# Optimization experiments

Hardware: AMD Instinct MI355X
Metric: run time of the kernel (lower is better)

The kernel has to match this reference:

```python
import jax, jax.numpy as jnp
import numpy as np

N, E, B = 150000, 600000, 1024
F_IN, F_HID = 78, 312          # 78 * 2**output_dim_power_0(=2)
OUT_DIM = 128
L, VOCAB, EMB = 1000, 26, 128  # num_features_xt+1 = 26 embedding rows
NF, KS = 8, 8                  # 2**n_filters_power, 2**kernel_size_power
CONV_FLAT = NF * (EMB - KS + 1)  # 8*121 = 968
K_HOPS = 2
SLOPE = 0.01                   # torch leaky_relu default

def _lin(k, i, o):
    s = 1.0 / np.sqrt(i)
    kw, kb = jax.random.split(k)
    return (jax.random.uniform(kw, (i, o), jnp.float32, -s, s),
            jax.random.uniform(kb, (o,), jnp.float32, -s, s))

def setup_inputs() -> dict:
    key = jax.random.key(0)
    ks = jax.random.split(key, 12)
    x = jax.random.normal(ks[0], (N, F_IN), jnp.float32)
    edge_index = jax.random.randint(ks[1], (2, E), 0, N)
    batch = (jnp.arange(N) * B) // N            # sorted graph ids, all B graphs nonempty
    target = jax.random.randint(ks[2], (B, L), 0, VOCAB)
    sgc_w, sgc_b = _lin(ks[3], F_IN, F_HID)
    fcg1_w, fcg1_b = _lin(ks[4], F_HID, OUT_DIM)
    emb_table = jax.random.normal(ks[5], (VOCAB, EMB), jnp.float32)
    sc = 1.0 / np.sqrt(L * KS)
    conv_w = jax.random.uniform(ks[6], (NF, L, KS), jnp.float32, -sc, sc)  # OIW
    conv_b = jax.random.uniform(ks[7], (NF,), jnp.float32, -sc, sc)
    fcxt_w, fcxt_b = _lin(ks[8], CONV_FLAT, OUT_DIM)
    fc1_w, fc1_b = _lin(ks[9], 2 * OUT_DIM, 1024)
    fc2_w, fc2_b = _lin(ks[10], 1024, 512)
    out_w, out_b = _lin(ks[11], 512, 1)
    return dict(x=x, sgc_w=sgc_w, sgc_b=sgc_b, fcg1_w=fcg1_w, fcg1_b=fcg1_b,
                emb_table=emb_table, conv_w=conv_w, conv_b=conv_b,
                fcxt_w=fcxt_w, fcxt_b=fcxt_b, fc1_w=fc1_w, fc1_b=fc1_b,
                fc2_w=fc2_w, fc2_b=fc2_b, out_w=out_w, out_b=out_b,
                edge_index=edge_index, batch=batch, target=target)

def reference(x, sgc_w, sgc_b, fcg1_w, fcg1_b, emb_table, conv_w, conv_b,
              fcxt_w, fcxt_b, fc1_w, fc1_b, fc2_w, fc2_b, out_w, out_b,
              edge_index, batch, target):
    # --- SGConv: K-hop symmetric-normalized propagation with self-loops, then linear ---
    loop = jnp.arange(N)
    src = jnp.concatenate([edge_index[0], loop])
    dst = jnp.concatenate([edge_index[1], loop])
    deg = jax.ops.segment_sum(jnp.ones_like(src, jnp.float32), dst, num_segments=N)
    dinv = jnp.where(deg > 0, jax.lax.rsqrt(deg), 0.0)
    norm = (dinv[src] * dinv[dst])[:, None]
    h = x
    for _ in range(K_HOPS):
        h = jax.ops.segment_sum(h[src] * norm, dst, num_segments=N)  # [N, F]
    h = jax.nn.leaky_relu(h @ sgc_w + sgc_b, SLOPE)                  # [N, 312]
    # --- global max pool per graph + fc_g1 ---
    g = jax.ops.segment_max(h, batch, num_segments=B)                # [B, 312]
    g = jax.nn.leaky_relu(g @ fcg1_w + fcg1_b, SLOPE)                # [B, 128]
    # --- protein branch: embed -> Conv1d(in=1000) over embed axis -> flatten -> fc ---
    emb = emb_table[target]                                          # [B, 1000, 128]
    conv = jax.lax.conv_general_dilated(emb, conv_w, (1,), 'VALID',
                                        dimension_numbers=('NCW', 'OIW', 'NCW'))
    conv = conv + conv_b[None, :, None]                              # [B, 8, 121]
    xt = conv.reshape(B, CONV_FLAT) @ fcxt_w + fcxt_b                # [B, 128]
    # --- head ---
    xc = jnp.concatenate([g, xt], axis=1)                            # [B, 256]
    xc = jax.nn.relu(xc @ fc1_w + fc1_b)
    xc = jax.nn.relu(xc @ fc2_w + fc2_b)
    return xc @ out_w + out_b                                        # [B, 1]
```

## Files before the change

kernel.cpp:

```cpp
#include <hip/hip_runtime.h>

#define N_NODES 150000
#define N_EDGES 600000
#define BATCH   1024
#define F_IN    78
#define F_HID   312
#define OUT_DIMW 128
#define SEQ_L   1000
#define VOCAB   26
#define EMB     128
#define NF      8
#define KS      8
#define CONV_WO 121
#define CONV_FLAT 968
#define SK      208
#define SLOPE   0.01f
#define KEY_NEGMAX ((int)0x80800000)
#define SCAN_NBLK ((N_NODES + 255) / 256)

#define KPU  96
#define NT   20
#define BSW_HALF (3 * NT * 64 * 8)
#define M_PAD 150016
#define HA_PLANE ((size_t)M_PAD * KPU)

typedef __attribute__((ext_vector_type(8))) short bf8;
typedef __attribute__((ext_vector_type(4))) float f4;

__device__ __forceinline__ short f2bf(float f) {
  unsigned u = __float_as_uint(f);
  return (short)((u + 0x7fffu + ((u >> 16) & 1u)) >> 16);
}
__device__ __forceinline__ float bf2f(short h) {
  return __uint_as_float(((unsigned)(unsigned short)h) << 16);
}

__device__ __forceinline__ int fkey(float v) {
  int i = __float_as_int(v);
  return i >= 0 ? i : (i ^ 0x7fffffff);
}
__device__ __forceinline__ float fdec(int k) {
  return __int_as_float(k >= 0 ? k : (k ^ 0x7fffffff));
}

__global__ void k_zero_i(int* __restrict__ p, int n) {
  int i = blockIdx.x * blockDim.x + threadIdx.x;
  if (i < n) p[i] = 0;
}

__global__ void k_deg(const int* __restrict__ dst, int* __restrict__ deg) {
  int e = blockIdx.x * blockDim.x + threadIdx.x;
  if (e < N_EDGES) atomicAdd(&deg[dst[e]], 1);
}

__global__ void k_dinv(const int* __restrict__ deg, float* __restrict__ dinv) {
  int i = blockIdx.x * blockDim.x + threadIdx.x;
  if (i < N_NODES) dinv[i] = rsqrtf((float)(deg[i] + 1));
}

__global__ __launch_bounds__(256) void k_scan1(const int* __restrict__ deg, int* __restrict__ rowptr,
                                               int* __restrict__ bsum) {
  __shared__ int s[256];
  int tid = threadIdx.x;
  int i = blockIdx.x * 256 + tid;
  int v = (i < N_NODES) ? deg[i] : 0;
  s[tid] = v;
  __syncthreads();
  int x = v;
  for (int o = 1; o < 256; o <<= 1) {
    int t = (tid >= o) ? s[tid - o] : 0;
    __syncthreads();
    x += t; s[tid] = x;
    __syncthreads();
  }
  if (i < N_NODES) rowptr[i] = x - v;
  if (tid == 255) bsum[blockIdx.x] = x;
}

__global__ __launch_bounds__(1024) void k_scan2(int* __restrict__ bsum) {
  __shared__ int s[1024];
  int tid = threadIdx.x;
  int v = (tid < SCAN_NBLK) ? bsum[tid] : 0;
  s[tid] = v;
  __syncthreads();
  int x = v;
  for (int o = 1; o < 1024; o <<= 1) {
    int t = (tid >= o) ? s[tid - o] : 0;
    __syncthreads();
    x += t; s[tid] = x;
    __syncthreads();
  }
  if (tid < SCAN_NBLK) bsum[tid] = x - v;
}

__global__ __launch_bounds__(256) void k_scan3(int* __restrict__ rowptr, const int* __restrict__ bsum,
                                               int* __restrict__ cnt) {
  int i = blockIdx.x * 256 + threadIdx.x;
  if (i < N_NODES) { rowptr[i] += bsum[blockIdx.x]; cnt[i] = 0; }
  if (i == 0) rowptr[N_NODES] = N_EDGES;
}

__global__ void k_fillcsr(const int* __restrict__ src, const int* __restrict__ dst,
                          const int* __restrict__ rowptr, int* __restrict__ cnt,
                          int* __restrict__ csr) {
  int e = blockIdx.x * blockDim.x + threadIdx.x;
  if (e < N_EDGES) {
    int d = dst[e];
    int pos = rowptr[d] + atomicAdd(&cnt[d], 1);
    csr[pos] = src[e];
  }
}

template<int HOP1>
__global__ __launch_bounds__(256) void k_pull(const int* __restrict__ rowptr,
                        const int* __restrict__ csr, const float* __restrict__ dinv,
                        const float* __restrict__ p, void* __restrict__ outv) {
  int dv = (int)((blockIdx.x * 256 + threadIdx.x) >> 6);
  if (dv >= N_NODES) return;
  int d = __builtin_amdgcn_readfirstlane(dv);
  int lane = threadIdx.x & 63;
  int j0 = rowptr[d], j1 = rowptr[d + 1];
  bool act = lane < 39;
  float dd = dinv[d];
  float2 aA = make_float2(0.f, 0.f), aB = aA, aC = aA, aD = aA;
  if (act) {
    float2 v = ((const float2*)(p + (size_t)d * F_IN))[lane];
    float c0 = HOP1 ? dd : 1.f;
    aA.x = c0 * v.x; aA.y = c0 * v.y;
  }
  int j = j0;
  for (; j + 3 < j1; j += 4) {
    int s0 = csr[j], s1 = csr[j + 1], s2 = csr[j + 2], s3 = csr[j + 3];
    float c0 = HOP1 ? dinv[s0] : 1.f, c1 = HOP1 ? dinv[s1] : 1.f;
    float c2 = HOP1 ? dinv[s2] : 1.f, c3 = HOP1 ? dinv[s3] : 1.f;
    if (act) {
      float2 u0 = ((const float2*)(p + (size_t)s0 * F_IN))[lane];
      float2 u1 = ((const float2*)(p + (size_t)s1 * F_IN))[lane];
      float2 u2 = ((const float2*)(p + (size_t)s2 * F_IN))[lane];
      float2 u3 = ((const float2*)(p + (size_t)s3 * F_IN))[lane];
      aA.x += c0 * u0.x; aA.y += c0 * u0.y;
      aB.x += c1 * u1.x; aB.y += c1 * u1.y;
      aC.x += c2 * u2.x; aC.y += c2 * u2.y;
      aD.x += c3 * u3.x; aD.y += c3 * u3.y;
    }
  }
  if (j + 1 < j1) {
    int s0 = csr[j], s1 = csr[j + 1];
    float c0 = HOP1 ? dinv[s0] : 1.f, c1 = HOP1 ? dinv[s1] : 1.f;
    if (act) {
      float2 u0 = ((const float2*)(p + (size_t)s0 * F_IN))[lane];
      float2 u1 = ((const float2*)(p + (size_t)s1 * F_IN))[lane];
      aA.x += c0 * u0.x; aA.y += c0 * u0.y;
      aB.x += c1 * u1.x; aB.y += c1 * u1.y;
    }
    j += 2;
  }
  if (j < j1) {
    int s0 = csr[j];
    float c0 = HOP1 ? dinv[s0] : 1.f;
    if (act) {
      float2 u0 = ((const float2*)(p + (size_t)s0 * F_IN))[lane];
      aC.x += c0 * u0.x; aC.y += c0 * u0.y;
    }
  }
  if (HOP1) {
    if (act) {
      float cs = dd * dd;
      ((float2*)((float*)outv + (size_t)d * F_IN))[lane] =
          make_float2(cs * (aA.x + aB.x + aC.x + aD.x), cs * (aA.y + aB.y + aC.y + aD.y));
    }
  } else {
    if (lane < 48) {
      float vx = dd * (aA.x + aB.x + aC.x + aD.x);
      float vy = dd * (aA.y + aB.y + aC.y + aD.y);
      short hx = f2bf(vx); short lx = f2bf(vx - bf2f(hx));
      short hy = f2bf(vy); short ly = f2bf(vy - bf2f(hy));
      short* hp = (short*)outv + (size_t)d * KPU;
      ((short2*)hp)[lane] = make_short2(hx, hy);
      ((short2*)(hp + HA_PLANE))[lane] = make_short2(lx, ly);
    }
  }
}

__global__ __launch_bounds__(256) void k_gemm_sk(const float* __restrict__ A, const float* __restrict__ B,
                        float* __restrict__ Cp, int M, int N, int K, int kc) {
  __shared__ float As[16][33];
  __shared__ float Bs[16][68];
  int bm = blockIdx.x * 32, bn = blockIdx.y * 64;
  int k0s = blockIdx.z * kc;
  int k1s = min(K, k0s + kc);
  int tid = threadIdx.x;
  int tx = tid & 15, ty = tid >> 4;
  float acc[2][4] = {};
  for (int k0 = k0s; k0 < k1s; k0 += 16) {
    {
      int i2 = tid * 2;
      int m = i2 >> 4, k = i2 & 15;
      float2 av = make_float2(0.f, 0.f);
      const float* Ap = A + (size_t)(bm + m) * K + k0 + k;
      if (k0 + k + 1 < k1s)      av = *(const float2*)Ap;
      else if (k0 + k < k1s)     av.x = Ap[0];
      As[k][m] = av.x; As[k + 1][m] = av.y;
    }
    {
      int i4 = tid * 4;
      int kr = i4 >> 6, n = i4 & 63;
      float4 bv = make_float4(0.f, 0.f, 0.f, 0.f);
      if (k0 + kr < k1s) bv = *(const float4*)(B + (size_t)(k0 + kr) * N + bn + n);
      *(float4*)&Bs[kr][n] = bv;
    }
    __syncthreads();
#pragma unroll
    for (int kk = 0; kk < 16; kk++) {
      float a0 = As[kk][ty * 2], a1 = As[kk][ty * 2 + 1];
      float4 b = *(const float4*)&Bs[kk][tx * 4];
      acc[0][0] += a0 * b.x; acc[0][1] += a0 * b.y; acc[0][2] += a0 * b.z; acc[0][3] += a0 * b.w;
      acc[1][0] += a1 * b.x; acc[1][1] += a1 * b.y; acc[1][2] += a1 * b.z; acc[1][3] += a1 * b.w;
    }
    __syncthreads();
  }
#pragma unroll
  for (int im = 0; im < 2; im++) {
    int m = bm + ty * 2 + im;
    float4 v = make_float4(acc[im][0], acc[im][1], acc[im][2], acc[im][3]);
    *(float4*)(Cp + ((size_t)blockIdx.z * M + m) * N + bn + tx * 4) = v;
  }
}

template<int ACT>
__global__ void k_sumact(const float* __restrict__ Cp, int S, const float* __restrict__ bias,
                         float* __restrict__ C, int nshift, int ldc, int coff) {
  int i = blockIdx.x * 256 + threadIdx.x;
  int MN = gridDim.x * 256;
  int m = i >> nshift, n = i & ((1 << nshift) - 1);
  float s = 0.f;
  for (int t = 0; t < S; t++) s += Cp[(size_t)t * MN + i];
  s += bias[n];
  if (ACT == 1) s = fmaxf(s, 0.f);
  if (ACT == 2) s = s > 0.f ? s : SLOPE * s;
  C[(size_t)m * ldc + coff + n] = s;
}

__global__ void k_bprep(const float* __restrict__ B, short* __restrict__ Bsw,
                        int* __restrict__ gkeys) {
  int i = blockIdx.x * 256 + threadIdx.x;
  if (i < BATCH * F_HID) gkeys[i] = KEY_NEGMAX;
  if (i >= BSW_HALF) return;
  int j = i & 7;
  int lane = (i >> 3) & 63;
  int rest = i >> 9;
  int nt = rest % NT, ksi = rest / NT;
  int n = nt * 16 + (lane & 15);
  int k = ksi * 32 + (lane >> 4) * 8 + j;
  float v = (k < F_IN && n < F_HID) ? B[k * F_HID + n] : 0.f;
  short h = f2bf(v);
  Bsw[i] = h;
  Bsw[BSW_HALF + i] = f2bf(v - bf2f(h));
}

__global__ __launch_bounds__(256) void k_gemm_max(const short* __restrict__ hA,
                           const short* __restrict__ Bsw,
                           const float* __restrict__ bias, int* __restrict__ gkeys) {
  __shared__ int red[2 * F_HID];
  int tid = threadIdx.x;
  int m0 = blockIdx.x * 64;

  for (int i = tid; i < 2 * F_HID; i += 256) red[i] = KEY_NEGMAX;
  __syncthreads();

  int w = tid >> 6, lane = tid & 63;
  int mrow = lane & 15, quad = lane >> 4;

  f4 acc[4][5];
#pragma unroll
  for (int mi = 0; mi < 4; mi++)
#pragma unroll
    for (int j = 0; j < 5; j++) acc[mi][j] = (f4)0.f;

#pragma unroll
  for (int ksi = 0; ksi < 3; ksi++) {
    bf8 ah[4], al[4];
#pragma unroll
    for (int mi = 0; mi < 4; mi++) {
      const short* ap = hA + (size_t)(m0 + mi * 16 + mrow) * KPU + ksi * 32 + quad * 8;
      ah[mi] = *(const bf8*)ap;
      al[mi] = *(const bf8*)(ap + HA_PLANE);
    }
    const short* bh = Bsw + ((size_t)(ksi * NT + w * 5) * 64 + lane) * 8;
    const short* bl = bh + BSW_HALF;
#pragma unroll
    for (int j = 0; j < 5; j++) {
      bf8 bhv = *(const bf8*)(bh + j * 512);
      bf8 blv = *(const bf8*)(bl + j * 512);
#pragma unroll
      for (int mi = 0; mi < 4; mi++) {
        acc[mi][j] = __builtin_amdgcn_mfma_f32_16x16x32_bf16(ah[mi], bhv, acc[mi][j], 0, 0, 0);
        acc[mi][j] = __builtin_amdgcn_mfma_f32_16x16x32_bf16(al[mi], bhv, acc[mi][j], 0, 0, 0);
        acc[mi][j] = __builtin_amdgcn_mfma_f32_16x16x32_bf16(ah[mi], blv, acc[mi][j], 0, 0, 0);
      }
    }
  }

  int g0 = (int)(((long long)m0 * BATCH) / N_NODES);
  int bnd = (int)((((long long)(g0 + 1)) * N_NODES + BATCH - 1) / BATCH);
#pragma unroll
  for (int j = 0; j < 5; j++) {
    int n = (w * 5 + j) * 16 + mrow;
    bool nok = n < F_HID;
    float bn = nok ? bias[n] : 0.f;
#pragma unroll
    for (int mi = 0; mi < 4; mi++) {
      int mb = m0 + mi * 16 + quad * 4;
      float mx0 = -3.4e38f, mx1 = -3.4e38f;
#pragma unroll
      for (int r = 0; r < 4; r++) {
        int m = mb + r;
        if (m >= N_NODES) continue;
        float v = acc[mi][j][r] + bn;
        v = v > 0.f ? v : SLOPE * v;
        if (m >= bnd) mx1 = fmaxf(mx1, v); else mx0 = fmaxf(mx0, v);
      }
      mx0 = fmaxf(mx0, __shfl_xor(mx0, 16, 64));
      mx0 = fmaxf(mx0, __shfl_xor(mx0, 32, 64));
      mx1 = fmaxf(mx1, __shfl_xor(mx1, 16, 64));
      mx1 = fmaxf(mx1, __shfl_xor(mx1, 32, 64));
      if (quad == 0 && nok) {
        if (mx0 > -3.3e38f) atomicMax(&red[n], fkey(mx0));
        if (mx1 > -3.3e38f) atomicMax(&red[F_HID + n], fkey(mx1));
      }
    }
  }
  __syncthreads();
  for (int i = tid; i < 2 * F_HID; i += 256) {
    int flag = i / F_HID, n = i - flag * F_HID;
    int g = g0 + flag;
    int key = red[i];
    if (g < BATCH && key != KEY_NEGMAX)
      atomicMax(&gkeys[g * F_HID + n], key);
  }
}

__global__ void k_decode(const int* __restrict__ gkeys, float* __restrict__ g, int n) {
  int i = blockIdx.x * blockDim.x + threadIdx.x;
  if (i < n) g[i] = fdec(gkeys[i]);
}

__global__ __launch_bounds__(256) void k_sbuild(const int* __restrict__ target, const float* __restrict__ conv_w,
                         float* __restrict__ Sg) {
  __shared__ int tl[SEQ_L];
  __shared__ unsigned short order[SEQ_L];
  __shared__ int cnt[VOCAB];
  __shared__ int off[VOCAB + 1];
  __shared__ float Sl[VOCAB * 64];
  int b = blockIdx.x, tid = threadIdx.x;
  for (int l = tid; l < SEQ_L; l += 256) tl[l] = target[b * SEQ_L + l];
  if (tid < VOCAB) cnt[tid] = 0;
  __syncthreads();
  for (int l = tid; l < SEQ_L; l += 256) atomicAdd(&cnt[tl[l]], 1);
  __syncthreads();
  if (tid == 0) { off[0] = 0; for (int v = 0; v < VOCAB; v++) off[v + 1] = off[v] + cnt[v]; }
  __syncthreads();
  if (tid < VOCAB) cnt[tid] = 0;
  __syncthreads();
  for (int l = tid; l < SEQ_L; l += 256) {
    int v = tl[l];
    int p = atomicAdd(&cnt[v], 1);
    order[off[v] + p] = (unsigned short)l;
  }
  for (int i = tid; i < VOCAB * 64; i += 256) Sl[i] = 0.f;
  __syncthreads();
  int fk = tid & 63, q = tid >> 6;
  int f = fk >> 3, k = fk & 7;
  const float* wp = conv_w + f * (SEQ_L * KS) + k;
  for (int v = 0; v < VOCAB; v++) {
    float acc = 0.f;
    for (int j = off[v] + q; j < off[v + 1]; j += 4) {
      int l = order[j];
      acc += wp[l * KS];
    }
    atomicAdd(&Sl[v * 64 + fk], acc);
  }
  __syncthreads();
  for (int i = tid; i < VOCAB * 64; i += 256) {
    int v = i >> 6, fk2 = i & 63;
    int ff = fk2 >> 3, kk = fk2 & 7;
    Sg[((size_t)b * NF + ff) * SK + v * KS + kk] = Sl[i];
  }
}

__global__ __launch_bounds__(256) void k_conv(const float* __restrict__ Sg, const float* __restrict__ emb,
                       const float* __restrict__ conv_b, float* __restrict__ convo) {
  __shared__ float Asub[32][SK];
  __shared__ float Etab[VOCAB * EMB];
  int r0 = blockIdx.x * 32;
  int tid = threadIdx.x;
  float* Af = &Asub[0][0];
  for (int i = tid; i < VOCAB * EMB; i += 256) Etab[i] = emb[i];
  for (int i = tid; i < 32 * SK; i += 256) Af[i] = Sg[(size_t)r0 * SK + i];
  __syncthreads();
  int w = tid & 127;
  int rg = tid >> 7;
  if (w < CONV_WO) {
    float acc[16] = {};
    for (int vk4 = 0; vk4 < SK; vk4 += 4) {
      int v0 = vk4 >> 3, k0 = vk4 & 7;
      float e0 = Etab[v0 * EMB + w + k0];
      float e1 = Etab[v0 * EMB + w + k0 + 1];
      float e2 = Etab[v0 * EMB + w + k0 + 2];
      float e3 = Etab[v0 * EMB + w + k0 + 3];
#pragma unroll
      for (int r = 0; r < 16; r++) {
        float4 a4 = *(const float4*)&Asub[rg * 16 + r][vk4];
        acc[r] += a4.x * e0 + a4.y * e1 + a4.z * e2 + a4.w * e3;
      }
    }
#pragma unroll
    for (int r = 0; r < 16; r++) {
      int row = r0 + rg * 16 + r;
      convo[(size_t)row * CONV_WO + w] = acc[r] + conv_b[row & 7];
    }
  }
}

__global__ void k_out(const float* __restrict__ a2, const float* __restrict__ w,
                      const float* __restrict__ b, float* __restrict__ out) {
  int row = (blockIdx.x * blockDim.x + threadIdx.x) >> 6;
  int lane = threadIdx.x & 63;
  if (row >= BATCH) return;
  const float* ar = a2 + (size_t)row * 512;
  float s = 0.f;
  for (int j = lane; j < 512; j += 64) s += ar[j] * w[j];
  for (int o = 32; o > 0; o >>= 1) s += __shfl_down(s, o, 64);
  if (lane == 0) out[row] = s + b[0];
}

extern "C" void kernel_launch(void* const* d_in, const int* in_sizes, int n_in,
                              void* d_out, int out_size, void* d_ws, size_t ws_size,
                              hipStream_t stream) {
  const float* x      = (const float*)d_in[0];
  const float* sgc_w  = (const float*)d_in[1];
  const float* sgc_b  = (const float*)d_in[2];
  const float* fcg1_w = (const float*)d_in[3];
  const float* fcg1_b = (const float*)d_in[4];
  const float* emb    = (const float*)d_in[5];
  const float* conv_w = (const float*)d_in[6];
  const float* conv_b = (const float*)d_in[7];
  const float* fcxt_w = (const float*)d_in[8];
  const float* fcxt_b = (const float*)d_in[9];
  const float* fc1_w  = (const float*)d_in[10];
  const float* fc1_b  = (const float*)d_in[11];
  const float* fc2_w  = (const float*)d_in[12];
  const float* fc2_b  = (const float*)d_in[13];
  const float* out_w  = (const float*)d_in[14];
  const float* out_b  = (const float*)d_in[15];
  const int* edge     = (const int*)d_in[16];
  const int* target   = (const int*)d_in[18];
  float* out = (float*)d_out;

  char* ws = (char*)d_ws;
  size_t off = 0;
  auto take = [&](size_t bytes) {
    void* p = ws + off;
    off += (bytes + 255) & ~(size_t)255;
    return p;
  };
  int*      deg    = (int*)     take((size_t)N_NODES * 4);
  float*    dinv   = (float*)   take((size_t)N_NODES * 4);
  int*      rowptr = (int*)     take((size_t)(N_NODES + 1) * 4);
  int*      bsum   = (int*)     take((size_t)SCAN_NBLK * 4);
  int*      cnt    = (int*)     take((size_t)N_NODES * 4);
  int*      csr    = (int*)     take((size_t)N_EDGES * 4);
  short*    hA     = (short*)   take((size_t)M_PAD * KPU * 4);
  float*    hB     = (float*)   take((size_t)N_NODES * F_IN * 4);
  short*    Bsw    = (short*)   take((size_t)2 * BSW_HALF * 2);
  int*      gkeys  = (int*)     take((size_t)BATCH * F_HID * 4);
  float*    gbuf   = (float*)   take((size_t)BATCH * F_HID * 4);
  float*    Sg     = (float*)   take((size_t)BATCH * NF * SK * 4);
  float*    convo  = (float*)   take((size_t)BATCH * NF * CONV_WO * 4);
  float*    xc     = (float*)   take((size_t)BATCH * 256 * 4);
  float*    a1     = (float*)   take((size_t)BATCH * 1024 * 4);
  float*    a2     = (float*)   take((size_t)BATCH * 512 * 4);
  float*    psum   = hB;

  const int* esrc = edge;
  const int* edst = edge + N_EDGES;

  k_zero_i<<<(N_NODES + 255) / 256, 256, 0, stream>>>(deg, N_NODES);
  k_deg<<<(N_EDGES + 255) / 256, 256, 0, stream>>>(edst, deg);
  k_dinv<<<(N_NODES + 255) / 256, 256, 0, stream>>>(deg, dinv);
  k_scan1<<<SCAN_NBLK, 256, 0, stream>>>(deg, rowptr, bsum);
  k_scan2<<<1, 1024, 0, stream>>>(bsum);
  k_scan3<<<SCAN_NBLK, 256, 0, stream>>>(rowptr, bsum, cnt);
  k_fillcsr<<<(N_EDGES + 255) / 256, 256, 0, stream>>>(esrc, edst, rowptr, cnt, csr);

  k_pull<1><<<(N_NODES * 64 + 255) / 256, 256, 0, stream>>>(rowptr, csr, dinv, x, hB);
  k_pull<0><<<(N_NODES * 64 + 255) / 256, 256, 0, stream>>>(rowptr, csr, dinv, hB, hA);

  k_bprep<<<(BATCH * F_HID + 255) / 256, 256, 0, stream>>>(sgc_w, Bsw, gkeys);
  k_gemm_max<<<M_PAD / 64, 256, 0, stream>>>(hA, Bsw, sgc_b, gkeys);
  k_decode<<<(BATCH * F_HID + 255) / 256, 256, 0, stream>>>(gkeys, gbuf, BATCH * F_HID);

  {
    dim3 g(BATCH / 32, OUT_DIMW / 64, 4);
    k_gemm_sk<<<g, 256, 0, stream>>>(gbuf, fcg1_w, psum, BATCH, OUT_DIMW, F_HID, 80);
    k_sumact<2><<<(BATCH * OUT_DIMW) / 256, 256, 0, stream>>>(psum, 4, fcg1_b, xc, 7, 256, 0);
  }

  k_sbuild<<<BATCH, 256, 0, stream>>>(target, conv_w, Sg);
  k_conv<<<(BATCH * NF) / 32, 256, 0, stream>>>(Sg, emb, conv_b, convo);
  {
    dim3 g(BATCH / 32, OUT_DIMW / 64, 8);
    k_gemm_sk<<<g, 256, 0, stream>>>(convo, fcxt_w, psum, BATCH, OUT_DIMW, CONV_FLAT, 128);
    k_sumact<0><<<(BATCH * OUT_DIMW) / 256, 256, 0, stream>>>(psum, 8, fcxt_b, xc, 7, 256, OUT_DIMW);
  }

  {
    dim3 g(BATCH / 32, 1024 / 64, 2);
    k_gemm_sk<<<g, 256, 0, stream>>>(xc, fc1_w, psum, BATCH, 1024, 256, 128);
    k_sumact<1><<<(BATCH * 1024) / 256, 256, 0, stream>>>(psum, 2, fc1_b, a1, 10, 1024, 0);
  }
  {
    dim3 g(BATCH / 32, 512 / 64, 4);
    k_gemm_sk<<<g, 256, 0, stream>>>(a1, fc2_w, psum, BATCH, 512, 1024, 256);
    k_sumact<1><<<(BATCH * 512) / 256, 256, 0, stream>>>(psum, 4, fc2_b, a2, 9, 512, 0);
  }
  k_out<<<(BATCH * 64) / 256, 256, 0, stream>>>(a2, out_w, out_b, out);
}
```

Measured before the change: 542.6 us.

## Interleave bf16 hi/lo split of propagated features and retile max-pool GEMM

The second propagation hop now writes each feature's bf16 high and low halves packed together in one 32-bit word, replacing the two separate planes. The pooled GEMM loads these packed words and unpacks them in registers. The GEMM is retiled to 512-thread blocks covering 128 rows and half of the output columns each, with a swizzled block order across 8 groups, and segment boundaries are computed per 16-row group. The aim is a single contiguous stream for the A operand and better locality, at the cost of extra unpack instructions and A rows being read by two blocks.

```diff
diff --git a/kernel.cpp b/kernel.cpp
--- a/kernel.cpp
+++ b/kernel.cpp
@@ -22,7 +22,8 @@
 #define NT   20
 #define BSW_HALF (3 * NT * 64 * 8)
 #define M_PAD 150016
-#define HA_PLANE ((size_t)M_PAD * KPU)
+#define GM_BLKS (M_PAD / 128 * 2)
+#define GM_CHUNK (GM_BLKS / 8)
 
 typedef __attribute__((ext_vector_type(8))) short bf8;
 typedef __attribute__((ext_vector_type(4))) float f4;
@@ -33,6 +34,11 @@
 }
 __device__ __forceinline__ float bf2f(short h) {
   return __uint_as_float(((unsigned)(unsigned short)h) << 16);
+}
+__device__ __forceinline__ unsigned packsplit(float v) {
+  short h = f2bf(v);
+  short l = f2bf(v - bf2f(h));
+  return ((unsigned)(unsigned short)h << 16) | (unsigned)(unsigned short)l;
 }
 
 __device__ __forceinline__ int fkey(float v) {
@@ -173,11 +179,8 @@
     if (lane < 48) {
       float vx = dd * (aA.x + aB.x + aC.x + aD.x);
       float vy = dd * (aA.y + aB.y + aC.y + aD.y);
-      short hx = f2bf(vx); short lx = f2bf(vx - bf2f(hx));
-      short hy = f2bf(vy); short ly = f2bf(vy - bf2f(hy));
-      short* hp = (short*)outv + (size_t)d * KPU;
-      ((short2*)hp)[lane] = make_short2(hx, hy);
-      ((short2*)(hp + HA_PLANE))[lane] = make_short2(lx, ly);
+      uint2 pk = make_uint2(packsplit(vx), packsplit(vy));
+      ((uint2*)((unsigned*)outv + (size_t)d * KPU))[lane] = pk;
     }
   }
 }
@@ -258,42 +261,57 @@
   Bsw[BSW_HALF + i] = f2bf(v - bf2f(h));
 }
 
-__global__ __launch_bounds__(256) void k_gemm_max(const short* __restrict__ hA,
+__global__ __launch_bounds__(512) void k_gemm_max(const unsigned* __restrict__ hAp,
                            const short* __restrict__ Bsw,
                            const float* __restrict__ bias, int* __restrict__ gkeys) {
   __shared__ int red[2 * F_HID];
   int tid = threadIdx.x;
-  int m0 = blockIdx.x * 64;
-
-  for (int i = tid; i < 2 * F_HID; i += 256) red[i] = KEY_NEGMAX;
+
+  int bid = blockIdx.x;
+  int swz = (bid & 7) * GM_CHUNK + (bid >> 3);
+  int mIdx = swz >> 1, nh2 = swz & 1;
+  int m0 = mIdx * 128;
+
+  for (int i = tid; i < 2 * F_HID; i += 512) red[i] = KEY_NEGMAX;
   __syncthreads();
 
   int w = tid >> 6, lane = tid & 63;
+  int mq = w & 3, nh = w >> 2;
+  int ntb = (nh2 * 2 + nh) * 5;
   int mrow = lane & 15, quad = lane >> 4;
 
-  f4 acc[4][5];
-#pragma unroll
-  for (int mi = 0; mi < 4; mi++)
+  f4 acc[2][5];
+#pragma unroll
+  for (int mi = 0; mi < 2; mi++)
 #pragma unroll
     for (int j = 0; j < 5; j++) acc[mi][j] = (f4)0.f;
 
+  const unsigned* apbase = hAp + (size_t)(m0 + mq * 32 + mrow) * KPU + quad * 8;
+  const short* bbase = Bsw + ((size_t)ntb * 64 + lane) * 8;
+
 #pragma unroll
   for (int ksi = 0; ksi < 3; ksi++) {
-    bf8 ah[4], al[4];
-#pragma unroll
-    for (int mi = 0; mi < 4; mi++) {
-      const short* ap = hA + (size_t)(m0 + mi * 16 + mrow) * KPU + ksi * 32 + quad * 8;
-      ah[mi] = *(const bf8*)ap;
-      al[mi] = *(const bf8*)(ap + HA_PLANE);
-    }
-    const short* bh = Bsw + ((size_t)(ksi * NT + w * 5) * 64 + lane) * 8;
+    bf8 ah[2], al[2];
+#pragma unroll
+    for (int mi = 0; mi < 2; mi++) {
+      const unsigned* ap = apbase + (size_t)mi * (16 * KPU) + ksi * 32;
+      uint4 u0 = *(const uint4*)ap;
+      uint4 u1 = *(const uint4*)(ap + 4);
+      unsigned uu[8] = {u0.x, u0.y, u0.z, u0.w, u1.x, u1.y, u1.z, u1.w};
+#pragma unroll
+      for (int j = 0; j < 8; j++) {
+        ah[mi][j] = (short)(uu[j] >> 16);
+        al[mi][j] = (short)(uu[j] & 0xffffu);
+      }
+    }
+    const short* bh = bbase + (size_t)ksi * (NT * 512);
     const short* bl = bh + BSW_HALF;
 #pragma unroll
     for (int j = 0; j < 5; j++) {
       bf8 bhv = *(const bf8*)(bh + j * 512);
       bf8 blv = *(const bf8*)(bl + j * 512);
 #pragma unroll
-      for (int mi = 0; mi < 4; mi++) {
+      for (int mi = 0; mi < 2; mi++) {
         acc[mi][j] = __builtin_amdgcn_mfma_f32_16x16x32_bf16(ah[mi], bhv, acc[mi][j], 0, 0, 0);
         acc[mi][j] = __builtin_amdgcn_mfma_f32_16x16x32_bf16(al[mi], bhv, acc[mi][j], 0, 0, 0);
         acc[mi][j] = __builtin_amdgcn_mfma_f32_16x16x32_bf16(ah[mi], blv, acc[mi][j], 0, 0, 0);
@@ -302,15 +320,18 @@
   }
 
   int g0 = (int)(((long long)m0 * BATCH) / N_NODES);
-  int bnd = (int)((((long long)(g0 + 1)) * N_NODES + BATCH - 1) / BATCH);
-#pragma unroll
-  for (int j = 0; j < 5; j++) {
-    int n = (w * 5 + j) * 16 + mrow;
-    bool nok = n < F_HID;
-    float bn = nok ? bias[n] : 0.f;
-#pragma unroll
-    for (int mi = 0; mi < 4; mi++) {
-      int mb = m0 + mi * 16 + quad * 4;
+#pragma unroll
+  for (int mi = 0; mi < 2; mi++) {
+    int mgrp = m0 + mq * 32 + mi * 16;
+    int gg  = (int)(((long long)mgrp * BATCH) / N_NODES);
+    int bndg = (int)((((long long)(gg + 1)) * N_NODES + BATCH - 1) / BATCH);
+    int s = gg - g0;
+    int mb = mgrp + quad * 4;
+#pragma unroll
+    for (int j = 0; j < 5; j++) {
+      int n = (ntb + j) * 16 + mrow;
+      bool nok = n < F_HID;
+      float bn = nok ? bias[n] : 0.f;
       float mx0 = -3.4e38f, mx1 = -3.4e38f;
 #pragma unroll
       for (int r = 0; r < 4; r++) {
@@ -318,20 +339,20 @@
         if (m >= N_NODES) continue;
         float v = acc[mi][j][r] + bn;
         v = v > 0.f ? v : SLOPE * v;
-        if (m >= bnd) mx1 = fmaxf(mx1, v); else mx0 = fmaxf(mx0, v);
+        if (m >= bndg) mx1 = fmaxf(mx1, v); else mx0 = fmaxf(mx0, v);
       }
       mx0 = fmaxf(mx0, __shfl_xor(mx0, 16, 64));
       mx0 = fmaxf(mx0, __shfl_xor(mx0, 32, 64));
       mx1 = fmaxf(mx1, __shfl_xor(mx1, 16, 64));
       mx1 = fmaxf(mx1, __shfl_xor(mx1, 32, 64));
       if (quad == 0 && nok) {
-        if (mx0 > -3.3e38f) atomicMax(&red[n], fkey(mx0));
-        if (mx1 > -3.3e38f) atomicMax(&red[F_HID + n], fkey(mx1));
+        if (mx0 > -3.3e38f) atomicMax(&red[s * F_HID + n], fkey(mx0));
+        if (mx1 > -3.3e38f && s == 0) atomicMax(&red[F_HID + n], fkey(mx1));
       }
     }
   }
   __syncthreads();
-  for (int i = tid; i < 2 * F_HID; i += 256) {
+  for (int i = tid; i < 2 * F_HID; i += 512) {
     int flag = i / F_HID, n = i - flag * F_HID;
     int g = g0 + flag;
     int key = red[i];
@@ -470,7 +491,7 @@
   int*      bsum   = (int*)     take((size_t)SCAN_NBLK * 4);
   int*      cnt    = (int*)     take((size_t)N_NODES * 4);
   int*      csr    = (int*)     take((size_t)N_EDGES * 4);
-  short*    hA     = (short*)   take((size_t)M_PAD * KPU * 4);
+  unsigned* hAp    = (unsigned*)take((size_t)M_PAD * KPU * 4);
   float*    hB     = (float*)   take((size_t)N_NODES * F_IN * 4);
   short*    Bsw    = (short*)   take((size_t)2 * BSW_HALF * 2);
   int*      gkeys  = (int*)     take((size_t)BATCH * F_HID * 4);
@@ -494,10 +515,10 @@
   k_fillcsr<<<(N_EDGES + 255) / 256, 256, 0, stream>>>(esrc, edst, rowptr, cnt, csr);
 
   k_pull<1><<<(N_NODES * 64 + 255) / 256, 256, 0, stream>>>(rowptr, csr, dinv, x, hB);
-  k_pull<0><<<(N_NODES * 64 + 255) / 256, 256, 0, stream>>>(rowptr, csr, dinv, hB, hA);
+  k_pull<0><<<(N_NODES * 64 + 255) / 256, 256, 0, stream>>>(rowptr, csr, dinv, hB, hAp);
 
   k_bprep<<<(BATCH * F_HID + 255) / 256, 256, 0, stream>>>(sgc_w, Bsw, gkeys);
-  k_gemm_max<<<M_PAD / 64, 256, 0, stream>>>(hA, Bsw, sgc_b, gkeys);
+  k_gemm_max<<<GM_BLKS, 512, 0, stream>>>(hAp, Bsw, sgc_b, gkeys);
   k_decode<<<(BATCH * F_HID + 255) / 256, 256, 0, stream>>>(gkeys, gbuf, BATCH * F_HID);
 
   {
```

Result: no change. 541.7 us (-0.2%).
